# Kernel tuning notes

Measured on AMD Instinct MI355X. Metric: run time of the kernel, lower is better.

The kernel has to match this reference:

```python
import jax, jax.numpy as jnp
import numpy as np

N, F_IN, HEADS, D_HEAD, HID, OUT, E = 50000, 128, 4, 64, 256, 2, 800000
NEG_SLOPE = 0.2


def setup_inputs() -> dict:
    key = jax.random.key(0)
    ks = jax.random.split(key, 12)
    x = jax.random.normal(ks[0], (N, F_IN), dtype=jnp.float32)
    edge_index = jax.random.randint(ks[1], (2, E), 0, N, dtype=jnp.int64)
    s = 0.05
    W_gat = jax.random.normal(ks[2], (F_IN, HEADS * D_HEAD), dtype=jnp.float32) * s
    att_src = jax.random.normal(ks[3], (HEADS, D_HEAD), dtype=jnp.float32) * s
    att_dst = jax.random.normal(ks[4], (HEADS, D_HEAD), dtype=jnp.float32) * s
    b_gat = jnp.zeros((HEADS * D_HEAD,), dtype=jnp.float32)
    W1 = jax.random.normal(ks[5], (HEADS * D_HEAD, HID), dtype=jnp.float32) * s
    b1 = jnp.zeros((HID,), dtype=jnp.float32)
    W2 = jax.random.normal(ks[6], (HID, HID), dtype=jnp.float32) * s
    b2 = jnp.zeros((HID,), dtype=jnp.float32)
    W3 = jax.random.normal(ks[7], (HID, OUT), dtype=jnp.float32) * s
    b3 = jnp.zeros((OUT,), dtype=jnp.float32)
    return {"x": x, "edge_index": edge_index, "W_gat": W_gat, "att_src": att_src,
            "att_dst": att_dst, "b_gat": b_gat, "W1": W1, "b1": b1,
            "W2": W2, "b2": b2, "W3": W3, "b3": b3}


def _gat(x, edge_index, W_gat, att_src, att_dst, b_gat):
    n = x.shape[0]
    loop = jnp.arange(n, dtype=edge_index.dtype)
    src = jnp.concatenate([edge_index[0], loop])  # [E+N] message sources j
    dst = jnp.concatenate([edge_index[1], loop])  # [E+N] message targets i
    h = (x @ W_gat).reshape(n, HEADS, D_HEAD)      # [N,H,D]
    a_s = jnp.einsum('nhd,hd->nh', h, att_src)     # [N,H]
    a_d = jnp.einsum('nhd,hd->nh', h, att_dst)     # [N,H]
    e = a_s[src] + a_d[dst]                        # [E',H]
    e = jax.nn.leaky_relu(e, NEG_SLOPE)
    # per-destination-node softmax over incoming edges (numerically stable)
    emax = jax.ops.segment_max(e, dst, num_segments=n)
    e = jnp.exp(e - emax[dst])
    denom = jax.ops.segment_sum(e, dst, num_segments=n)
    alpha = e / denom[dst]                         # [E',H]
    msg = h[src] * alpha[:, :, None]               # [E',H,D]
    out = jax.ops.segment_sum(msg, dst, num_segments=n)  # [N,H,D]
    return out.reshape(n, HEADS * D_HEAD) + b_gat


def reference(x, edge_index, W_gat, att_src, att_dst, b_gat, W1, b1, W2, b2, W3, b3):
    h = _gat(x, edge_index, W_gat, att_src, att_dst, b_gat)
    h = jax.nn.relu(h @ W1 + b1)
    h = jax.nn.relu(h @ W2 + b2)
    return h @ W3 + b3
```

## Files before the change

kernel.cpp:

```cpp
#include <hip/hip_runtime.h>
#include <math.h>

#define N_NODES 50000
#define NP 50048
#define F_IN 128
#define HD 256
#define HID 256
#define NE 800000
#define CAP 64
#define NEG_SLOPE 0.2f
#define G1_BLOCKS (NP / 64)
#define FILL_BLOCKS ((NE + 1023) / 1024)
#define CNT_STRIDE 16

typedef __attribute__((ext_vector_type(8))) __bf16 bf16x8;
typedef __attribute__((ext_vector_type(4))) __bf16 bf16x4;
typedef __attribute__((ext_vector_type(4))) float f32x4;

#define GLD_LDS16(g, l)                                                      \
    __builtin_amdgcn_global_load_lds(                                        \
        (const __attribute__((address_space(1))) unsigned int*)(g),          \
        (__attribute__((address_space(3))) unsigned int*)(l), 16, 0, 0)

__device__ __forceinline__ void store_u16_wt(unsigned short* p, unsigned v) {
    unsigned long long a = (unsigned long long)p;
    asm volatile("global_store_short %0, %1, off sc0 sc1" :: "v"(a), "v"(v) : "memory");
}

#define PB_INIT 196
#define PB_WG   128
#define PB_W1   256
#define PB_W2   256

__global__ __launch_bounds__(256) void prep_kernel(const float* __restrict__ Wg,
                                                   const float* __restrict__ W1,
                                                   const float* __restrict__ W2,
                                                   __bf16* __restrict__ Wg_t,
                                                   __bf16* __restrict__ W1_t,
                                                   __bf16* __restrict__ W2_t,
                                                   int* __restrict__ cnt,
                                                   unsigned short* __restrict__ bucket) {
    int b = blockIdx.x, t = threadIdx.x;
    if (b < PB_INIT) {
        int n = b * 256 + t;
        if (n < N_NODES) { cnt[(size_t)n * CNT_STRIDE] = 1; bucket[n * CAP] = (unsigned short)n; }
    } else if (b < PB_INIT + PB_WG) {
        int i = (b - PB_INIT) * 256 + t;
        int m = i >> 7, k = i & 127;
        Wg_t[i] = (__bf16)Wg[(size_t)k * HD + m];
    } else if (b < PB_INIT + PB_WG + PB_W1) {
        int i = (b - PB_INIT - PB_WG) * 256 + t;
        int m = i >> 8, k = i & 255;
        W1_t[i] = (__bf16)W1[(size_t)k * HID + m];
    } else {
        int i = (b - PB_INIT - PB_WG - PB_W1) * 256 + t;
        int m = i >> 8, k = i & 255;
        W2_t[i] = (__bf16)W2[(size_t)k * HID + m];
    }
}

__global__ __launch_bounds__(256) void g1_fill_kernel(const float* __restrict__ x,
                                                      const __bf16* __restrict__ Bt,
                                                      const float* __restrict__ att_src,
                                                      const float* __restrict__ att_dst,
                                                      const int* __restrict__ ew,
                                                      __bf16* __restrict__ h,
                                                      float* __restrict__ a_s,
                                                      float* __restrict__ a_d,
                                                      int* __restrict__ cnt,
                                                      unsigned short* __restrict__ bucket) {
    __shared__ __bf16 As[64 * 32];
    __shared__ __bf16 Bs[256 * 32];

    if (blockIdx.x >= G1_BLOCKS) {
        const int base = (blockIdx.x - G1_BLOCKS) * 1024 + threadIdx.x;
        const int e0 = base, e1 = base + 256, e2 = base + 512, e3 = base + 768;
        const bool v0 = e0 < NE, v1 = e1 < NE, v2 = e2 < NE, v3 = e3 < NE;
        long long p0 = 0, p1 = 0, p2 = 0, p3 = 0;
        if (v0) p0 = *(const long long*)&ew[2 * e0];
        if (v1) p1 = *(const long long*)&ew[2 * e1];
        if (v2) p2 = *(const long long*)&ew[2 * e2];
        if (v3) p3 = *(const long long*)&ew[2 * e3];
        const int hiall = (int)(p0 >> 32) | (int)(p1 >> 32) |
                          (int)(p2 >> 32) | (int)(p3 >> 32);
        unsigned long long bal = __ballot(hiall != 0);
        int s0 = 0, s1 = 0, s2 = 0, s3 = 0, d0 = 0, d1 = 0, d2 = 0, d3 = 0;
        if (bal == 0) {
            s0 = (int)p0; s1 = (int)p1; s2 = (int)p2; s3 = (int)p3;
            if (v0) d0 = ew[2 * NE + 2 * e0];
            if (v1) d1 = ew[2 * NE + 2 * e1];
            if (v2) d2 = ew[2 * NE + 2 * e2];
            if (v3) d3 = ew[2 * NE + 2 * e3];
        } else {
            if (v0) { s0 = ew[e0]; d0 = ew[NE + e0]; }
            if (v1) { s1 = ew[e1]; d1 = ew[NE + e1]; }
            if (v2) { s2 = ew[e2]; d2 = ew[NE + e2]; }
            if (v3) { s3 = ew[e3]; d3 = ew[NE + e3]; }
        }
        int pos0 = CAP, pos1 = CAP, pos2 = CAP, pos3 = CAP;
        if (v0) pos0 = atomicAdd(&cnt[(size_t)d0 * CNT_STRIDE], 1);
        if (v1) pos1 = atomicAdd(&cnt[(size_t)d1 * CNT_STRIDE], 1);
        if (v2) pos2 = atomicAdd(&cnt[(size_t)d2 * CNT_STRIDE], 1);
        if (v3) pos3 = atomicAdd(&cnt[(size_t)d3 * CNT_STRIDE], 1);
        if (pos0 < CAP) store_u16_wt(&bucket[d0 * CAP + pos0], (unsigned)(unsigned short)s0);
        if (pos1 < CAP) store_u16_wt(&bucket[d1 * CAP + pos1], (unsigned)(unsigned short)s1);
        if (pos2 < CAP) store_u16_wt(&bucket[d2 * CAP + pos2], (unsigned)(unsigned short)s2);
        if (pos3 < CAP) store_u16_wt(&bucket[d3 * CAP + pos3], (unsigned)(unsigned short)s3);
        return;
    }

    const int t = threadIdx.x;
    const int lane = t & 63, wv = t >> 6;
    const int lr = lane & 15, q = lane >> 4, lk = q * 8;
    const int col_off = wv * 64;
    const int row0 = blockIdx.x * 64;
    const int sr = t >> 2, sk = (t & 3) * 8;
    const int arow = row0 + sr;
    const bool avalid = arow < N_NODES;

    f32x4 acc[4][4];
#pragma unroll
    for (int r = 0; r < 4; ++r)
#pragma unroll
        for (int c = 0; c < 4; ++c) acc[r][c] = f32x4{0.f, 0.f, 0.f, 0.f};

    for (int k0 = 0; k0 < F_IN; k0 += 32) {
        float4 v0 = {0, 0, 0, 0}, v1 = {0, 0, 0, 0};
        if (avalid) {
            const float* xp = &x[(size_t)arow * F_IN + k0 + sk];
            v0 = *(const float4*)xp;
            v1 = *(const float4*)(xp + 4);
        }
        bf16x8 o;
        o[0] = (__bf16)v0.x; o[1] = (__bf16)v0.y; o[2] = (__bf16)v0.z; o[3] = (__bf16)v0.w;
        o[4] = (__bf16)v1.x; o[5] = (__bf16)v1.y; o[6] = (__bf16)v1.z; o[7] = (__bf16)v1.w;
        *(bf16x8*)&As[sr * 32 + sk] = o;
#pragma unroll
        for (int s = 0; s < 4; ++s) {
            int r = s * 64 + sr;
            GLD_LDS16(&Bt[(size_t)r * F_IN + k0 + sk], &Bs[r * 32 + sk]);
        }
        __syncthreads();
        bf16x8 af[4], bfr[4];
#pragma unroll
        for (int i = 0; i < 4; ++i) {
            af[i]  = *(const bf16x8*)&As[(i * 16 + lr) * 32 + lk];
            bfr[i] = *(const bf16x8*)&Bs[(col_off + i * 16 + lr) * 32 + lk];
        }
#pragma unroll
        for (int r = 0; r < 4; ++r)
#pragma unroll
            for (int c = 0; c < 4; ++c)
                acc[r][c] = __builtin_amdgcn_mfma_f32_16x16x32_bf16(af[r], bfr[c], acc[r][c], 0, 0, 0);
        __syncthreads();
    }

    float asv[4], adv[4];
#pragma unroll
    for (int c = 0; c < 4; ++c) {
        int col = col_off + c * 16 + lr;
        asv[c] = att_src[col];
        adv[c] = att_dst[col];
    }
    float ps[4][4], pd[4][4];
#pragma unroll
    for (int r = 0; r < 4; ++r)
#pragma unroll
        for (int i = 0; i < 4; ++i) { ps[r][i] = 0.f; pd[r][i] = 0.f; }

#pragma unroll
    for (int c = 0; c < 4; ++c) {
        int col = col_off + c * 16 + lr;
#pragma unroll
        for (int r = 0; r < 4; ++r) {
#pragma unroll
            for (int i = 0; i < 4; ++i) {
                int row = row0 + r * 16 + q * 4 + i;
                float v = acc[r][c][i];
                h[(size_t)row * HD + col] = (__bf16)v;
                ps[r][i] += v * asv[c];
                pd[r][i] += v * adv[c];
            }
        }
    }
#pragma unroll
    for (int r = 0; r < 4; ++r)
#pragma unroll
        for (int i = 0; i < 4; ++i) {
#pragma unroll
            for (int m = 1; m < 16; m <<= 1) {
                ps[r][i] += __shfl_xor(ps[r][i], m);
                pd[r][i] += __shfl_xor(pd[r][i], m);
            }
        }
    if (lr == 0) {
#pragma unroll
        for (int r = 0; r < 4; ++r)
#pragma unroll
            for (int i = 0; i < 4; ++i) {
                int row = row0 + r * 16 + q * 4 + i;
                a_s[row * 4 + wv] = ps[r][i];
                a_d[row * 4 + wv] = pd[r][i];
            }
    }
}

__device__ __forceinline__ float lrelu(float v) { return v >= 0.f ? v : NEG_SLOPE * v; }

__global__ __launch_bounds__(64) void gat_aggregate_kernel(const __bf16* __restrict__ h,
                                                           const float* __restrict__ a_s,
                                                           const float* __restrict__ a_d,
                                                           const int* __restrict__ cnt,
                                                           const unsigned short* __restrict__ bucket,
                                                           const float* __restrict__ b_gat,
                                                           __bf16* __restrict__ gat) {
    __shared__ unsigned short s_src[64];
    __shared__ float s_alpha[64][4];
    const int lane = threadIdx.x;
    const int n = blockIdx.x;

    int deg = cnt[(size_t)n * CNT_STRIDE];
    if (deg > CAP) deg = CAP;
    int src = n;
    float4 ad = *(const float4*)&a_d[n * 4];
    float4 as4 = {0, 0, 0, 0};
    if (lane < deg) {
        src = bucket[n * CAP + lane];
        as4 = *(const float4*)&a_s[src * 4];
    }

    const int half = lane >> 5;
    const int l32 = lane & 31;
    const int c0 = l32 * 8;
    const int head = l32 >> 3;
    const int pj0 = __shfl(src, half);
    const int pj1 = __shfl(src, 2 + half);
    const int pj2 = __shfl(src, 4 + half);
    const int pj3 = __shfl(src, 6 + half);
    const bf16x8 hp0 = *(const bf16x8*)&h[(size_t)pj0 * HD + c0];
    const bf16x8 hp1 = *(const bf16x8*)&h[(size_t)pj1 * HD + c0];
    const bf16x8 hp2 = *(const bf16x8*)&h[(size_t)pj2 * HD + c0];
    const bf16x8 hp3 = *(const bf16x8*)&h[(size_t)pj3 * HD + c0];

    float4 e = {-1e30f, -1e30f, -1e30f, -1e30f};
    if (lane < deg) {
        e.x = lrelu(as4.x + ad.x);
        e.y = lrelu(as4.y + ad.y);
        e.z = lrelu(as4.z + ad.z);
        e.w = lrelu(as4.w + ad.w);
    }
    float4 m = e;
#pragma unroll
    for (int off = 1; off < 64; off <<= 1) {
        m.x = fmaxf(m.x, __shfl_xor(m.x, off));
        m.y = fmaxf(m.y, __shfl_xor(m.y, off));
        m.z = fmaxf(m.z, __shfl_xor(m.z, off));
        m.w = fmaxf(m.w, __shfl_xor(m.w, off));
    }
    float4 wgt = {0, 0, 0, 0};
    if (lane < deg) {
        wgt.x = __expf(e.x - m.x); wgt.y = __expf(e.y - m.y);
        wgt.z = __expf(e.z - m.z); wgt.w = __expf(e.w - m.w);
    }
    float4 s = wgt;
#pragma unroll
    for (int off = 1; off < 64; off <<= 1) {
        s.x += __shfl_xor(s.x, off); s.y += __shfl_xor(s.y, off);
        s.z += __shfl_xor(s.z, off); s.w += __shfl_xor(s.w, off);
    }
    s_src[lane] = (unsigned short)src;
    s_alpha[lane][0] = wgt.x / s.x;
    s_alpha[lane][1] = wgt.y / s.y;
    s_alpha[lane][2] = wgt.z / s.z;
    s_alpha[lane][3] = wgt.w / s.w;
    __syncthreads();

    float acc[8];
#pragma unroll
    for (int k = 0; k < 8; ++k) acc[k] = 0.f;

    const int mde = (deg + 1) & ~1;
    int j = 0;
    if (mde >= 8) {
        const float a0 = s_alpha[half][head];
        const float a1 = s_alpha[2 + half][head];
        const float a2 = s_alpha[4 + half][head];
        const float a3 = s_alpha[6 + half][head];
#pragma unroll
        for (int k = 0; k < 8; ++k)
            acc[k] += a0 * (float)hp0[k] + a1 * (float)hp1[k]
                    + a2 * (float)hp2[k] + a3 * (float)hp3[k];
        j = 8;
        for (; j + 8 <= mde; j += 8) {
            int j0 = j + half, j1 = j + 2 + half, j2 = j + 4 + half, j3 = j + 6 + half;
            int s0 = s_src[j0], s1 = s_src[j1], s2 = s_src[j2], s3 = s_src[j3];
            float b0 = s_alpha[j0][head], b1 = s_alpha[j1][head];
            float b2 = s_alpha[j2][head], b3 = s_alpha[j3][head];
            bf16x8 h0 = *(const bf16x8*)&h[(size_t)s0 * HD + c0];
            bf16x8 h1 = *(const bf16x8*)&h[(size_t)s1 * HD + c0];
            bf16x8 h2 = *(const bf16x8*)&h[(size_t)s2 * HD + c0];
            bf16x8 h3 = *(const bf16x8*)&h[(size_t)s3 * HD + c0];
#pragma unroll
            for (int k = 0; k < 8; ++k)
                acc[k] += b0 * (float)h0[k] + b1 * (float)h1[k]
                        + b2 * (float)h2[k] + b3 * (float)h3[k];
        }
    }
    for (; j < mde; j += 2) {
        int j0 = j + half;
        int s0 = s_src[j0];
        float a0 = s_alpha[j0][head];
        bf16x8 h0 = *(const bf16x8*)&h[(size_t)s0 * HD + c0];
#pragma unroll
        for (int k = 0; k < 8; ++k)
            acc[k] += a0 * (float)h0[k];
    }
#pragma unroll
    for (int k = 0; k < 8; ++k) acc[k] += __shfl_xor(acc[k], 32);

    if (half == 0) {
        float4 bg0 = *(const float4*)&b_gat[c0];
        float4 bg1 = *(const float4*)&b_gat[c0 + 4];
        bf16x8 o;
        o[0] = (__bf16)(acc[0] + bg0.x); o[1] = (__bf16)(acc[1] + bg0.y);
        o[2] = (__bf16)(acc[2] + bg0.z); o[3] = (__bf16)(acc[3] + bg0.w);
        o[4] = (__bf16)(acc[4] + bg1.x); o[5] = (__bf16)(acc[5] + bg1.y);
        o[6] = (__bf16)(acc[6] + bg1.z); o[7] = (__bf16)(acc[7] + bg1.w);
        *(bf16x8*)&gat[(size_t)n * HD + c0] = o;
    }
}

__global__ __launch_bounds__(256) void fused_mlp_kernel(const __bf16* __restrict__ A,
                                                        const __bf16* __restrict__ W1t,
                                                        const __bf16* __restrict__ W2t,
                                                        const float* __restrict__ b1,
                                                        const float* __restrict__ b2,
                                                        const float* __restrict__ W3,
                                                        const float* __restrict__ b3,
                                                        float* __restrict__ out) {
    __shared__ __bf16 As[64 * 32];
    __shared__ __bf16 Ws[256 * 32];
    __shared__ __bf16 h1s[8 * 64 * 32];
    __shared__ float s_out[64][2];
    const int t = threadIdx.x;
    const int lane = t & 63, wv = t >> 6;
    const int lr = lane & 15, q = lane >> 4, lk = q * 8;
    const int col_off = wv * 64;
    const int row0 = blockIdx.x * 64;
    const int sr = t >> 2, sk = (t & 3) * 8;

    if (t < 128) ((float*)s_out)[t] = 0.f;

    f32x4 acc[4][4];
#pragma unroll
    for (int r = 0; r < 4; ++r)
#pragma unroll
        for (int c = 0; c < 4; ++c) acc[r][c] = f32x4{0.f, 0.f, 0.f, 0.f};

    for (int k0 = 0; k0 < HD; k0 += 32) {
        GLD_LDS16(&A[(size_t)(row0 + sr) * HD + k0 + sk], &As[sr * 32 + sk]);
#pragma unroll
        for (int s = 0; s < 4; ++s) {
            int r = s * 64 + sr;
            GLD_LDS16(&W1t[(size_t)r * HD + k0 + sk], &Ws[r * 32 + sk]);
        }
        __syncthreads();
        bf16x8 af[4], bfr[4];
#pragma unroll
        for (int i = 0; i < 4; ++i) {
            af[i]  = *(const bf16x8*)&As[(i * 16 + lr) * 32 + lk];
            bfr[i] = *(const bf16x8*)&Ws[(col_off + i * 16 + lr) * 32 + lk];
        }
#pragma unroll
        for (int r = 0; r < 4; ++r)
#pragma unroll
            for (int c = 0; c < 4; ++c)
                acc[r][c] = __builtin_amdgcn_mfma_f32_16x16x32_bf16(af[r], bfr[c], acc[r][c], 0, 0, 0);
        __syncthreads();
    }
#pragma unroll
    for (int c = 0; c < 4; ++c) {
        int col = col_off + c * 16 + lr;
        float bv = b1[col];
        int cb = (col >> 5) * 2048;
        int kk = col & 31;
#pragma unroll
        for (int r = 0; r < 4; ++r)
#pragma unroll
            for (int i = 0; i < 4; ++i) {
                int row = r * 16 + q * 4 + i;
                float v = fmaxf(acc[r][c][i] + bv, 0.f);
                h1s[cb + row * 32 + kk] = (__bf16)v;
                acc[r][c][i] = 0.f;
            }
    }
    __syncthreads();

    for (int k0 = 0; k0 < HID; k0 += 32) {
#pragma unroll
        for (int s = 0; s < 4; ++s) {
            int r = s * 64 + sr;
            GLD_LDS16(&W2t[(size_t)r * HID + k0 + sk], &Ws[r * 32 + sk]);
        }
        __syncthreads();
        const int cb = (k0 >> 5) * 2048;
        bf16x8 af[4], bfr[4];
#pragma unroll
        for (int i = 0; i < 4; ++i) {
            af[i]  = *(const bf16x8*)&h1s[cb + (i * 16 + lr) * 32 + lk];
            bfr[i] = *(const bf16x8*)&Ws[(col_off + i * 16 + lr) * 32 + lk];
        }
#pragma unroll
        for (int r = 0; r < 4; ++r)
#pragma unroll
            for (int c = 0; c < 4; ++c)
                acc[r][c] = __builtin_amdgcn_mfma_f32_16x16x32_bf16(af[r], bfr[c], acc[r][c], 0, 0, 0);
        __syncthreads();
    }

    float b2v[4], w30[4], w31[4];
#pragma unroll
    for (int c = 0; c < 4; ++c) {
        int col = col_off + c * 16 + lr;
        b2v[c] = b2[col];
        w30[c] = W3[col * 2];
        w31[c] = W3[col * 2 + 1];
    }
#pragma unroll
    for (int r = 0; r < 4; ++r) {
#pragma unroll
        for (int i = 0; i < 4; ++i) {
            float o0 = 0.f, o1 = 0.f;
#pragma unroll
            for (int c = 0; c < 4; ++c) {
                float v = fmaxf(acc[r][c][i] + b2v[c], 0.f);
                o0 += v * w30[c];
                o1 += v * w31[c];
            }
#pragma unroll
            for (int m = 1; m < 16; m <<= 1) {
                o0 += __shfl_xor(o0, m);
                o1 += __shfl_xor(o1, m);
            }
            if (lr == 0) {
                int row = r * 16 + q * 4 + i;
                atomicAdd(&s_out[row][0], o0);
                atomicAdd(&s_out[row][1], o1);
            }
        }
    }
    __syncthreads();
    if (t < 128) {
        int row = t >> 1, o = t & 1;
        int g = row0 + row;
        if (g < N_NODES) out[g * 2 + o] = s_out[row][o] + b3[o];
    }
}

extern "C" void kernel_launch(void* const* d_in, const int* in_sizes, int n_in,
                              void* d_out, int out_size, void* d_ws, size_t ws_size,
                              hipStream_t stream) {
    const float* x       = (const float*)d_in[0];
    const int*   ei      = (const int*)d_in[1];
    const float* W_gat   = (const float*)d_in[2];
    const float* att_src = (const float*)d_in[3];
    const float* att_dst = (const float*)d_in[4];
    const float* b_gat   = (const float*)d_in[5];
    const float* W1      = (const float*)d_in[6];
    const float* b1      = (const float*)d_in[7];
    const float* W2      = (const float*)d_in[8];
    const float* b2      = (const float*)d_in[9];
    const float* W3      = (const float*)d_in[10];
    const float* b3      = (const float*)d_in[11];
    float* out = (float*)d_out;

    char* ws = (char*)d_ws;
    __bf16* h_bf   = (__bf16*)ws;  ws += (size_t)NP * HD * 2;
    __bf16* gat_bf = (__bf16*)ws;  ws += (size_t)NP * HD * 2;
    __bf16* Wg_t   = (__bf16*)ws;  ws += (size_t)HD * F_IN * 2;
    __bf16* W1_t   = (__bf16*)ws;  ws += (size_t)HID * HD * 2;
    __bf16* W2_t   = (__bf16*)ws;  ws += (size_t)HID * HID * 2;
    float* a_s     = (float*)ws;   ws += (size_t)NP * 4 * 4;
    float* a_d     = (float*)ws;   ws += (size_t)NP * 4 * 4;
    int* cnt       = (int*)ws;     ws += (size_t)N_NODES * CNT_STRIDE * 4;
    unsigned short* bucket = (unsigned short*)ws;
    ws += (size_t)N_NODES * CAP * 2;

    prep_kernel<<<PB_INIT + PB_WG + PB_W1 + PB_W2, 256, 0, stream>>>(
        W_gat, W1, W2, Wg_t, W1_t, W2_t, cnt, bucket);
    g1_fill_kernel<<<G1_BLOCKS + FILL_BLOCKS, 256, 0, stream>>>(
        x, Wg_t, att_src, att_dst, ei, h_bf, a_s, a_d, cnt, bucket);
    gat_aggregate_kernel<<<N_NODES, 64, 0, stream>>>(h_bf, a_s, a_d, cnt, bucket,
                                                     b_gat, gat_bf);
    fused_mlp_kernel<<<NP / 64, 256, 0, stream>>>(gat_bf, W1_t, W2_t, b1, b2, W3, b3, out);
}
```

Measured before the change: 242.7 us.

## Fold weight prep and self-loop init into the fill/GEMM kernel, drop prep launch

Removes the separate prep kernel. Self-loop entries are now inserted by the edge-fill path as extra items, and the counters are zeroed with a memset. The W1/W2 bf16 transposes run as extra blocks of the fused g1_fill kernel. The GAT projection GEMM now reads fp32 W_gat directly with strided loads and converts it in place, instead of loading a pre-transposed bf16 copy via global_load_lds. This saves a kernel launch but makes the B-tile loads uncoalesced and duplicated across all GEMM blocks. Self-loops no longer sit in slot 0 of each bucket, which could change the order in which each node's neighbours are summed.

```diff
diff --git a/kernel.cpp b/kernel.cpp
--- a/kernel.cpp
+++ b/kernel.cpp
@@ -10,7 +10,9 @@
 #define CAP 64
 #define NEG_SLOPE 0.2f
 #define G1_BLOCKS (NP / 64)
-#define FILL_BLOCKS ((NE + 1023) / 1024)
+#define NITEMS (NE + N_NODES)
+#define FILL_BLOCKS ((NITEMS + 1023) / 1024)
+#define WT_BLOCKS 512
 #define CNT_STRIDE 16
 
 typedef __attribute__((ext_vector_type(8))) __bf16 bf16x8;
@@ -27,81 +29,73 @@
     asm volatile("global_store_short %0, %1, off sc0 sc1" :: "v"(a), "v"(v) : "memory");
 }
 
-#define PB_INIT 196
-#define PB_WG   128
-#define PB_W1   256
-#define PB_W2   256
-
-__global__ __launch_bounds__(256) void prep_kernel(const float* __restrict__ Wg,
-                                                   const float* __restrict__ W1,
-                                                   const float* __restrict__ W2,
-                                                   __bf16* __restrict__ Wg_t,
-                                                   __bf16* __restrict__ W1_t,
-                                                   __bf16* __restrict__ W2_t,
-                                                   int* __restrict__ cnt,
-                                                   unsigned short* __restrict__ bucket) {
-    int b = blockIdx.x, t = threadIdx.x;
-    if (b < PB_INIT) {
-        int n = b * 256 + t;
-        if (n < N_NODES) { cnt[(size_t)n * CNT_STRIDE] = 1; bucket[n * CAP] = (unsigned short)n; }
-    } else if (b < PB_INIT + PB_WG) {
-        int i = (b - PB_INIT) * 256 + t;
-        int m = i >> 7, k = i & 127;
-        Wg_t[i] = (__bf16)Wg[(size_t)k * HD + m];
-    } else if (b < PB_INIT + PB_WG + PB_W1) {
-        int i = (b - PB_INIT - PB_WG) * 256 + t;
-        int m = i >> 8, k = i & 255;
-        W1_t[i] = (__bf16)W1[(size_t)k * HID + m];
-    } else {
-        int i = (b - PB_INIT - PB_WG - PB_W1) * 256 + t;
-        int m = i >> 8, k = i & 255;
-        W2_t[i] = (__bf16)W2[(size_t)k * HID + m];
-    }
-}
-
 __global__ __launch_bounds__(256) void g1_fill_kernel(const float* __restrict__ x,
-                                                      const __bf16* __restrict__ Bt,
+                                                      const float* __restrict__ Wg,
                                                       const float* __restrict__ att_src,
                                                       const float* __restrict__ att_dst,
                                                       const int* __restrict__ ew,
+                                                      const float* __restrict__ W1,
+                                                      const float* __restrict__ W2,
                                                       __bf16* __restrict__ h,
                                                       float* __restrict__ a_s,
                                                       float* __restrict__ a_d,
                                                       int* __restrict__ cnt,
-                                                      unsigned short* __restrict__ bucket) {
+                                                      unsigned short* __restrict__ bucket,
+                                                      __bf16* __restrict__ W1_t,
+                                                      __bf16* __restrict__ W2_t) {
     __shared__ __bf16 As[64 * 32];
     __shared__ __bf16 Bs[256 * 32];
+
+    if (blockIdx.x >= G1_BLOCKS + FILL_BLOCKS) {
+        int b = blockIdx.x - G1_BLOCKS - FILL_BLOCKS;
+        int t = threadIdx.x;
+        if (b < 256) {
+            int i = b * 256 + t;
+            int m = i >> 8, k = i & 255;
+            W1_t[i] = (__bf16)W1[(size_t)k * HID + m];
+        } else {
+            int i = (b - 256) * 256 + t;
+            int m = i >> 8, k = i & 255;
+            W2_t[i] = (__bf16)W2[(size_t)k * HID + m];
+        }
+        return;
+    }
 
     if (blockIdx.x >= G1_BLOCKS) {
         const int base = (blockIdx.x - G1_BLOCKS) * 1024 + threadIdx.x;
         const int e0 = base, e1 = base + 256, e2 = base + 512, e3 = base + 768;
-        const bool v0 = e0 < NE, v1 = e1 < NE, v2 = e2 < NE, v3 = e3 < NE;
+        const bool a0 = e0 < NITEMS, a1 = e1 < NITEMS, a2 = e2 < NITEMS, a3 = e3 < NITEMS;
+        const bool i0 = e0 < NE, i1 = e1 < NE, i2 = e2 < NE, i3 = e3 < NE;
         long long p0 = 0, p1 = 0, p2 = 0, p3 = 0;
-        if (v0) p0 = *(const long long*)&ew[2 * e0];
-        if (v1) p1 = *(const long long*)&ew[2 * e1];
-        if (v2) p2 = *(const long long*)&ew[2 * e2];
-        if (v3) p3 = *(const long long*)&ew[2 * e3];
+        if (i0) p0 = *(const long long*)&ew[2 * e0];
+        if (i1) p1 = *(const long long*)&ew[2 * e1];
+        if (i2) p2 = *(const long long*)&ew[2 * e2];
+        if (i3) p3 = *(const long long*)&ew[2 * e3];
         const int hiall = (int)(p0 >> 32) | (int)(p1 >> 32) |
                           (int)(p2 >> 32) | (int)(p3 >> 32);
         unsigned long long bal = __ballot(hiall != 0);
         int s0 = 0, s1 = 0, s2 = 0, s3 = 0, d0 = 0, d1 = 0, d2 = 0, d3 = 0;
         if (bal == 0) {
             s0 = (int)p0; s1 = (int)p1; s2 = (int)p2; s3 = (int)p3;
-            if (v0) d0 = ew[2 * NE + 2 * e0];
-            if (v1) d1 = ew[2 * NE + 2 * e1];
-            if (v2) d2 = ew[2 * NE + 2 * e2];
-            if (v3) d3 = ew[2 * NE + 2 * e3];
+            if (i0) d0 = ew[2 * NE + 2 * e0];
+            if (i1) d1 = ew[2 * NE + 2 * e1];
+            if (i2) d2 = ew[2 * NE + 2 * e2];
+            if (i3) d3 = ew[2 * NE + 2 * e3];
         } else {
-            if (v0) { s0 = ew[e0]; d0 = ew[NE + e0]; }
-            if (v1) { s1 = ew[e1]; d1 = ew[NE + e1]; }
-            if (v2) { s2 = ew[e2]; d2 = ew[NE + e2]; }
-            if (v3) { s3 = ew[e3]; d3 = ew[NE + e3]; }
-        }
+            if (i0) { s0 = ew[e0]; d0 = ew[NE + e0]; }
+            if (i1) { s1 = ew[e1]; d1 = ew[NE + e1]; }
+            if (i2) { s2 = ew[e2]; d2 = ew[NE + e2]; }
+            if (i3) { s3 = ew[e3]; d3 = ew[NE + e3]; }
+        }
+        if (a0 && !i0) { s0 = d0 = e0 - NE; }
+        if (a1 && !i1) { s1 = d1 = e1 - NE; }
+        if (a2 && !i2) { s2 = d2 = e2 - NE; }
+        if (a3 && !i3) { s3 = d3 = e3 - NE; }
         int pos0 = CAP, pos1 = CAP, pos2 = CAP, pos3 = CAP;
-        if (v0) pos0 = atomicAdd(&cnt[(size_t)d0 * CNT_STRIDE], 1);
-        if (v1) pos1 = atomicAdd(&cnt[(size_t)d1 * CNT_STRIDE], 1);
-        if (v2) pos2 = atomicAdd(&cnt[(size_t)d2 * CNT_STRIDE], 1);
-        if (v3) pos3 = atomicAdd(&cnt[(size_t)d3 * CNT_STRIDE], 1);
+        if (a0) pos0 = atomicAdd(&cnt[(size_t)d0 * CNT_STRIDE], 1);
+        if (a1) pos1 = atomicAdd(&cnt[(size_t)d1 * CNT_STRIDE], 1);
+        if (a2) pos2 = atomicAdd(&cnt[(size_t)d2 * CNT_STRIDE], 1);
+        if (a3) pos3 = atomicAdd(&cnt[(size_t)d3 * CNT_STRIDE], 1);
         if (pos0 < CAP) store_u16_wt(&bucket[d0 * CAP + pos0], (unsigned)(unsigned short)s0);
         if (pos1 < CAP) store_u16_wt(&bucket[d1 * CAP + pos1], (unsigned)(unsigned short)s1);
         if (pos2 < CAP) store_u16_wt(&bucket[d2 * CAP + pos2], (unsigned)(unsigned short)s2);
@@ -117,6 +111,8 @@
     const int sr = t >> 2, sk = (t & 3) * 8;
     const int arow = row0 + sr;
     const bool avalid = arow < N_NODES;
+    const int br = t >> 2;
+    const int bq = (t & 3) * 8;
 
     f32x4 acc[4][4];
 #pragma unroll
@@ -136,9 +132,13 @@
         o[4] = (__bf16)v1.x; o[5] = (__bf16)v1.y; o[6] = (__bf16)v1.z; o[7] = (__bf16)v1.w;
         *(bf16x8*)&As[sr * 32 + sk] = o;
 #pragma unroll
-        for (int s = 0; s < 4; ++s) {
-            int r = s * 64 + sr;
-            GLD_LDS16(&Bt[(size_t)r * F_IN + k0 + sk], &Bs[r * 32 + sk]);
+        for (int s2 = 0; s2 < 4; ++s2) {
+            const int rowb = s2 * 64 + br;
+            const float* wp = &Wg[(size_t)(k0 + bq) * HD + rowb];
+            bf16x8 ob;
+#pragma unroll
+            for (int i = 0; i < 8; ++i) ob[i] = (__bf16)wp[(size_t)i * HD];
+            *(bf16x8*)&Bs[rowb * 32 + bq] = ob;
         }
         __syncthreads();
         bf16x8 af[4], bfr[4];
@@ -477,7 +477,6 @@
     char* ws = (char*)d_ws;
     __bf16* h_bf   = (__bf16*)ws;  ws += (size_t)NP * HD * 2;
     __bf16* gat_bf = (__bf16*)ws;  ws += (size_t)NP * HD * 2;
-    __bf16* Wg_t   = (__bf16*)ws;  ws += (size_t)HD * F_IN * 2;
     __bf16* W1_t   = (__bf16*)ws;  ws += (size_t)HID * HD * 2;
     __bf16* W2_t   = (__bf16*)ws;  ws += (size_t)HID * HID * 2;
     float* a_s     = (float*)ws;   ws += (size_t)NP * 4 * 4;
@@ -486,10 +485,10 @@
     unsigned short* bucket = (unsigned short*)ws;
     ws += (size_t)N_NODES * CAP * 2;
 
-    prep_kernel<<<PB_INIT + PB_WG + PB_W1 + PB_W2, 256, 0, stream>>>(
-        W_gat, W1, W2, Wg_t, W1_t, W2_t, cnt, bucket);
-    g1_fill_kernel<<<G1_BLOCKS + FILL_BLOCKS, 256, 0, stream>>>(
-        x, Wg_t, att_src, att_dst, ei, h_bf, a_s, a_d, cnt, bucket);
+    hipMemsetAsync(cnt, 0, (size_t)N_NODES * CNT_STRIDE * 4, stream);
+    g1_fill_kernel<<<G1_BLOCKS + FILL_BLOCKS + WT_BLOCKS, 256, 0, stream>>>(
+        x, W_gat, att_src, att_dst, ei, W1, W2, h_bf, a_s, a_d, cnt, bucket,
+        W1_t, W2_t);
     gat_aggregate_kernel<<<N_NODES, 64, 0, stream>>>(h_bf, a_s, a_d, cnt, bucket,
                                                      b_gat, gat_bf);
     fused_mlp_kernel<<<NP / 64, 256, 0, stream>>>(gat_bf, W1_t, W2_t, b1, b2, W3, b3, out);
```

New measurement: 246.7 us. About the same (+1.6%).
